# Optimization experiments

Measured on AMD Instinct MI355X. Metric: run time of the kernel, lower is better.

Reference implementation:

```python
import jax, jax.numpy as jnp
import numpy as np

B, NQ, NC1, NC2 = 2, 1024, 1024, 1024
QD = CD1 = CD2 = 1024
H, DH = 8, 64
INNER = H * DH          # 512
VD = 1024               # v_dim, split across heads -> 128 per head
VDH = VD // H


def setup_inputs() -> dict:
    key = jax.random.key(0)
    ks = jax.random.split(key, 18)
    f = lambda k, shape: jax.random.normal(k, shape, jnp.float32) * 0.02
    return {
        "x": f(ks[0], (B, NQ, QD)),
        "context": f(ks[1], (B, NC1, CD1)),
        "context2": f(ks[2], (B, NC2, CD2)),
        "mask1": jax.random.uniform(ks[3], (B, NQ, NC1)) > 0.1,
        "mask2": jax.random.uniform(ks[4], (B, NQ, NC2)) > 0.1,
        "Wq": f(ks[5], (QD, INNER)),  "bq": f(ks[6], (INNER,)),
        "Wk1": f(ks[7], (CD1, INNER)), "bk1": f(ks[8], (INNER,)),
        "Wv1": f(ks[9], (CD1, VD)),    "bv1": f(ks[10], (VD,)),
        "Wk2": f(ks[11], (CD2, INNER)), "bk2": f(ks[12], (INNER,)),
        "Wv2": f(ks[13], (CD2, VD)),    "bv2": f(ks[14], (VD,)),
        "Wo": f(ks[15], (VD, VD)),      "bo": f(ks[16], (VD,)),
    }


def _split_heads(t, d):
    # b n (h d) -> b h n d
    b, n, _ = t.shape
    return t.reshape(b, n, H, d).transpose(0, 2, 1, 3)


def reference(x, context, context2, mask1, mask2,
              Wq, bq, Wk1, bk1, Wv1, bv1, Wk2, bk2, Wv2, bv2, Wo, bo):
    scale = DH ** -0.5
    q = x @ Wq + bq
    k = jnp.concatenate([context @ Wk1 + bk1, context2 @ Wk2 + bk2], axis=1)
    v = jnp.concatenate([context @ Wv1 + bv1, context2 @ Wv2 + bv2], axis=1)

    qh = _split_heads(q, DH)   # [B,H,NQ,DH]
    kh = _split_heads(k, DH)   # [B,H,NC1+NC2,DH]
    vh = _split_heads(v, VDH)  # [B,H,NC1+NC2,VDH]

    sim = jnp.einsum('bhid,bhjd->bhij', qh, kh) * scale  # [B,H,NQ,J]
    mask = jnp.concatenate([mask1, mask2], axis=2)[:, None, :, :]  # [B,1,NQ,J]
    max_neg = -jnp.finfo(sim.dtype).max
    sim = jnp.where(mask, sim, max_neg)

    attn = jax.nn.softmax(sim, axis=-1)
    out = jnp.einsum('bhij,bhjd->bhid', attn, vh)          # [B,H,NQ,VDH]
    out = out.transpose(0, 2, 1, 3).reshape(B, NQ, VD)     # b n (h d)
    return out @ Wo + bo
```

## Files before the change

kernel.cpp:

```cpp
#include <hip/hip_runtime.h>
#include <math.h>

typedef short bf16x8 __attribute__((ext_vector_type(8)));
typedef float f32x4  __attribute__((ext_vector_type(4)));

__device__ __forceinline__ unsigned short f2bf(float f) {
    unsigned int u = __builtin_bit_cast(unsigned int, f);
    u += 0x7FFFu + ((u >> 16) & 1u);
    return (unsigned short)(u >> 16);
}
__device__ __forceinline__ float bf2f(unsigned short u) {
    return __builtin_bit_cast(float, (unsigned int)u << 16);
}
__device__ __forceinline__ unsigned pktrunc(float hi, float lo) {
    return __builtin_amdgcn_perm(__builtin_bit_cast(unsigned, hi),
                                 __builtin_bit_cast(unsigned, lo), 0x07060302u);
}

__device__ __forceinline__ void gld16(const unsigned short* g, unsigned short* l) {
    __builtin_amdgcn_global_load_lds(
        (const __attribute__((address_space(1))) void*)g,
        (__attribute__((address_space(3))) void*)l, 16, 0, 0);
}

#define QSCALE 0.18033688011112042f

__global__ __launch_bounds__(256) void prep(
    const float* __restrict__ x, const float* __restrict__ c1, const float* __restrict__ c2,
    const int* __restrict__ mask1, const int* __restrict__ mask2,
    const float* __restrict__ Wq, const float* __restrict__ Wk1, const float* __restrict__ Wk2,
    const float* __restrict__ Wv1, const float* __restrict__ Wv2, const float* __restrict__ Wo,
    unsigned short* __restrict__ xb, unsigned short* __restrict__ c1b, unsigned short* __restrict__ c2b,
    unsigned short* __restrict__ Wqt, unsigned short* __restrict__ Wk1t, unsigned short* __restrict__ Wk2t,
    unsigned short* __restrict__ Wv1t, unsigned short* __restrict__ Wv2t, unsigned short* __restrict__ Wot,
    unsigned long long* __restrict__ mpk)
{
    __shared__ float T[64][65];
    const int bid = blockIdx.x, t = threadIdx.x;

    if (bid < 3072) {
        const int z = bid >> 10;
        const float* a = z == 0 ? x : (z == 1 ? c1 : c2);
        unsigned short* o = z == 0 ? xb : (z == 1 ? c1b : c2b);
        size_t i = ((size_t)(bid & 1023) * 256 + t) * 8;
        float4 x0 = *(const float4*)&a[i];
        float4 x1 = *(const float4*)&a[i + 4];
        uint4 pk;
        pk.x = (unsigned)f2bf(x0.x) | ((unsigned)f2bf(x0.y) << 16);
        pk.y = (unsigned)f2bf(x0.z) | ((unsigned)f2bf(x0.w) << 16);
        pk.z = (unsigned)f2bf(x1.x) | ((unsigned)f2bf(x1.y) << 16);
        pk.w = (unsigned)f2bf(x1.z) | ((unsigned)f2bf(x1.w) << 16);
        *(uint4*)&o[i] = pk;
        return;
    }
    if (bid < 4224) {
        const float* W; unsigned short* O; int N, n0, k0; bool perm = false;
        if (bid < 3456) {
            int l = bid - 3072, z = l >> 7, rem = l & 127;
            W = z == 0 ? Wq : (z == 1 ? Wk1 : Wk2);
            O = z == 0 ? Wqt : (z == 1 ? Wk1t : Wk2t);
            N = 512; n0 = (rem & 7) << 6; k0 = (rem >> 3) << 6;
        } else {
            int l = bid - 3456, z = l >> 8, rem = l & 255;
            W = z == 0 ? Wv1 : (z == 1 ? Wv2 : Wo);
            O = z == 0 ? Wv1t : (z == 1 ? Wv2t : Wot);
            N = 1024; n0 = (rem & 15) << 6; k0 = (rem >> 4) << 6;
            perm = (z == 2);
        }
        #pragma unroll
        for (int i = 0; i < 4; i++) {
            int vi = t + (i << 8);
            int r = vi >> 4, c4 = (vi & 15) << 2;
            *(float4*)&T[r][c4] = *(const float4*)&W[(size_t)(k0 + r) * N + n0 + c4];
        }
        __syncthreads();
        #pragma unroll
        for (int i = 0; i < 4; i++) {
            int vi = t + (i << 8);
            int n = vi >> 4, k4 = (vi & 15) << 2;
            if (!perm) {
                uint2 pk;
                pk.x = (unsigned)f2bf(T[k4 + 0][n]) | ((unsigned)f2bf(T[k4 + 1][n]) << 16);
                pk.y = (unsigned)f2bf(T[k4 + 2][n]) | ((unsigned)f2bf(T[k4 + 3][n]) << 16);
                *(uint2*)&O[(size_t)(n0 + n) * 1024 + k0 + k4] = pk;
            } else {
                #pragma unroll
                for (int ii = 0; ii < 4; ii++) {
                    int k = k0 + k4 + ii, f = k & 127;
                    int kp = (k & ~127) | ((f & 15) << 3) | (f >> 4);
                    O[(size_t)(n0 + n) * 1024 + kp] = f2bf(T[k4 + ii][n]);
                }
            }
        }
        return;
    }
    {
        int wid = ((bid - 4224) << 2) + (t >> 6);
        int lane = t & 63;
        const int* m1 = mask1 + ((size_t)wid << 10);
        const int* m2 = mask2 + ((size_t)wid << 10);
        unsigned long long* o = mpk + ((size_t)wid << 5);
        #pragma unroll
        for (int win = 0; win < 16; win++) {
            unsigned long long bal = __ballot(m1[(win << 6) + lane] != 0);
            if (lane == 0) o[win] = bal;
        }
        #pragma unroll
        for (int win = 0; win < 16; win++) {
            unsigned long long bal = __ballot(m2[(win << 6) + lane] != 0);
            if (lane == 0) o[16 + win] = bal;
        }
    }
}

template<int NT>
__device__ __forceinline__ void gemm_core(
    const unsigned short* __restrict__ A,
    const unsigned short* __restrict__ Wt,
    int K, int gm0, int gn0,
    unsigned short (*As)[32], unsigned short (*Bs)[32],
    f32x4 (&acc)[4][NT / 32])
{
    constexpr int NS = NT / 32;
    const int t = threadIdx.x;
    const int lane = t & 63, w = t >> 6;
    const int wm = (w & 1) << 6, wn = (w >> 1) * (NT / 2);
    const int l15 = lane & 15, quad = lane >> 4;

    for (int k0 = 0; k0 < K; k0 += 32) {
        __syncthreads();
        #pragma unroll
        for (int i = 0; i < 2; i++) {
            int r0 = (i << 6) + (w << 4);
            int ra = r0 + (lane >> 2);
            int kc = (lane & 3) << 3;
            gld16(&A[(size_t)(gm0 + ra) * K + k0 + kc], &As[r0][0] + ((size_t)lane << 3));
        }
        #pragma unroll
        for (int i = 0; i < NT / 64; i++) {
            int r0 = (i << 6) + (w << 4);
            int ra = r0 + (lane >> 2);
            int kc = (lane & 3) << 3;
            gld16(&Wt[(size_t)(gn0 + ra) * K + k0 + kc], &Bs[r0][0] + ((size_t)lane << 3));
        }
        __syncthreads();
        bf16x8 af[4], bg[NS];
        #pragma unroll
        for (int i = 0; i < 4; i++)
            af[i] = *(const bf16x8*)&As[wm + (i << 4) + l15][quad << 3];
        #pragma unroll
        for (int j = 0; j < NS; j++)
            bg[j] = *(const bf16x8*)&Bs[wn + (j << 4) + l15][quad << 3];
        #pragma unroll
        for (int i = 0; i < 4; i++)
            #pragma unroll
            for (int j = 0; j < NS; j++)
                acc[i][j] = __builtin_amdgcn_mfma_f32_16x16x32_bf16(af[i], bg[j], acc[i][j], 0, 0, 0);
    }
}

__global__ __launch_bounds__(256) void proj_all(
    const unsigned short* __restrict__ xb, const unsigned short* __restrict__ c1b,
    const unsigned short* __restrict__ c2b,
    const unsigned short* __restrict__ Wqt, const unsigned short* __restrict__ Wk1t,
    const unsigned short* __restrict__ Wk2t, const unsigned short* __restrict__ Wv1t,
    const unsigned short* __restrict__ Wv2t,
    const float* __restrict__ bq, const float* __restrict__ bk1, const float* __restrict__ bk2,
    const float* __restrict__ bv1, const float* __restrict__ bv2,
    unsigned short* __restrict__ qbuf, unsigned short* __restrict__ khb,
    unsigned short* __restrict__ vhb)
{
    __shared__ unsigned short smem[17408];
    unsigned short (*As)[32] = (unsigned short(*)[32])smem;
    unsigned short (*Bs)[32] = (unsigned short(*)[32])(smem + 4096);
    unsigned short* Ts = smem;

    const int bid = blockIdx.x;
    int z, bx, by;
    if (bid < 192) { z = bid >> 6; int l = bid & 63; by = l >> 2; bx = l & 3; }
    else { int l = bid - 192; z = 3 + (l >> 7); l &= 127; by = l >> 3; bx = l & 7; }
    const unsigned short* A  = (z == 0) ? xb : (z == 1 || z == 3) ? c1b : c2b;
    const unsigned short* Wt = (z == 0) ? Wqt : (z == 1) ? Wk1t : (z == 2) ? Wk2t
                             : (z == 3) ? Wv1t : Wv2t;
    const float* bias = (z == 0) ? bq : (z == 1) ? bk1 : (z == 2) ? bk2
                      : (z == 3) ? bv1 : bv2;
    const int gm0 = by << 7, gn0 = bx << 7;

    f32x4 acc[4][4];
    #pragma unroll
    for (int i = 0; i < 4; i++)
        #pragma unroll
        for (int j = 0; j < 4; j++) acc[i][j] = (f32x4){0.f, 0.f, 0.f, 0.f};

    gemm_core<128>(A, Wt, 1024, gm0, gn0, As, Bs, acc);

    const int t = threadIdx.x;
    const int lane = t & 63, w = t >> 6;
    const int wm = (w & 1) << 6, wn = (w >> 1) << 6;
    const int l15 = lane & 15, quad = lane >> 4;
    float bb[4];
    #pragma unroll
    for (int j = 0; j < 4; j++) bb[j] = bias[gn0 + wn + (j << 4) + l15];

    if (z == 0) {
        #pragma unroll
        for (int i = 0; i < 4; i++) {
            int mb = gm0 + wm + (i << 4) + (quad << 2);
            #pragma unroll
            for (int p = 0; p < 4; p++)
                #pragma unroll
                for (int j = 0; j < 4; j++)
                    qbuf[(size_t)(mb + p) * 512 + gn0 + wn + (j << 4) + l15]
                        = f2bf((acc[i][j][p] + bb[j]) * QSCALE);
        }
        return;
    }

    __syncthreads();
    const int b = gm0 >> 10;
    if (z < 3) {
        const int jb = ((z == 2) ? 1024 : 0) + (gm0 & 1023);
        #pragma unroll
        for (int i = 0; i < 4; i++) {
            int jl0 = wm + (i << 4) + (quad << 2);
            #pragma unroll
            for (int j = 0; j < 4; j++) {
                int n = wn + (j << 4) + l15;
                #pragma unroll
                for (int p = 0; p < 4; p++)
                    Ts[(jl0 + p) * 136 + n] = f2bf(acc[i][j][p] + bb[j]);
            }
        }
        __syncthreads();
        #pragma unroll
        for (int rr = 0; rr < 8; rr++) {
            int row = (rr << 4) + (t >> 4), cd = t & 15;
            uint4 v = *(const uint4*)&Ts[row * 136 + (cd << 3)];
            int jg = jb + row;
            int hcol = (gn0 >> 6) + (cd >> 3);
            size_t hb = ((size_t)((b << 3) + hcol) << 17);
            *(uint4*)&khb[hb + ((size_t)jg << 6) + ((((cd & 7) ^ (jg & 7))) << 3)] = v;
        }
    } else {
        const int jb = ((z == 3) ? 0 : 1024) + (gm0 & 1023);
        #pragma unroll
        for (int i = 0; i < 4; i++) {
            int jl0 = wm + (i << 4) + (quad << 2);
            #pragma unroll
            for (int j = 0; j < 4; j++) {
                int n = wn + (j << 4) + l15;
                unsigned long long pk = 0;
                #pragma unroll
                for (int p = 0; p < 4; p++)
                    pk |= (unsigned long long)f2bf(acc[i][j][p] + bb[j]) << (16 * p);
                *(unsigned long long*)&Ts[n * 136 + jl0] = pk;
            }
        }
        __syncthreads();
        const int hv = gn0 >> 7;
        size_t hbase = ((size_t)((b << 3) + hv) << 18);
        #pragma unroll
        for (int rr = 0; rr < 8; rr++) {
            int f = (rr << 4) + (t >> 4), cj = t & 15;
            uint4 v = *(const uint4*)&Ts[f * 136 + (cj << 3)];
            int jj = jb + (cj << 3);
            int jpos = (jj & ~63) | ((((jj >> 3) & 7) ^ (f & 7)) << 3);
            *(uint4*)&vhb[hbase + ((size_t)f << 11) + jpos] = v;
        }
    }
}

__global__ __launch_bounds__(256) void gemm_out(
    const unsigned short* __restrict__ abuf, const unsigned short* __restrict__ Wot,
    const float* __restrict__ bo, float* __restrict__ out)
{
    __shared__ unsigned short As[128][32];
    __shared__ unsigned short Bs[64][32];
    const int gm0 = blockIdx.y << 7, gn0 = blockIdx.x << 6;

    f32x4 acc[4][2];
    #pragma unroll
    for (int i = 0; i < 4; i++)
        #pragma unroll
        for (int j = 0; j < 2; j++) acc[i][j] = (f32x4){0.f, 0.f, 0.f, 0.f};

    gemm_core<64>(abuf, Wot, 1024, gm0, gn0, As, Bs, acc);

    const int lane = threadIdx.x & 63, w = threadIdx.x >> 6;
    const int wm = (w & 1) << 6, wn = (w >> 1) << 5;
    const int l15 = lane & 15, quad = lane >> 4;
    float bb[2];
    #pragma unroll
    for (int j = 0; j < 2; j++) bb[j] = bo[gn0 + wn + (j << 4) + l15];
    #pragma unroll
    for (int i = 0; i < 4; i++) {
        int mb = gm0 + wm + (i << 4) + (quad << 2);
        #pragma unroll
        for (int p = 0; p < 4; p++)
            #pragma unroll
            for (int j = 0; j < 2; j++)
                out[(size_t)(mb + p) * 1024 + gn0 + wn + (j << 4) + l15] = acc[i][j][p] + bb[j];
    }
}

__global__ __launch_bounds__(256) void attn_mfma(
    const unsigned short* __restrict__ qbuf, const unsigned short* __restrict__ khb,
    const unsigned short* __restrict__ vhb, const unsigned long long* __restrict__ mpk,
    unsigned short* __restrict__ Opart, float* __restrict__ ml)
{
    __shared__ unsigned short Ks[64 * 64];
    __shared__ unsigned short VsT[128 * 64];
    __shared__ unsigned short Ps[64 * 64];

    const int t = threadIdx.x;
    const int bid = blockIdx.x;
    const int hs = bid >> 8, r = bid & 255;
    const int h = r & 7, qt = (r >> 3) & 15, b = r >> 7;
    const int q0 = qt << 6;
    const int lane = t & 63, w = t >> 6, l15 = lane & 15, quad = lane >> 4;
    const int v7 = l15 & 7;

    const unsigned short* qrow = qbuf + (((size_t)(b << 10) + q0 + (w << 4) + l15) << 9) + (h << 6);
    const bf16x8 aq0 = *(const bf16x8*)&qrow[quad << 3];
    const bf16x8 aq1 = *(const bf16x8*)&qrow[32 + (quad << 3)];

    f32x4 acc[8];
    #pragma unroll
    for (int ct = 0; ct < 8; ct++) acc[ct] = (f32x4){0.f, 0.f, 0.f, 0.f};
    float m_l = -3.0e38f, l_l = 0.f;

    const unsigned short* kh = khb + ((size_t)((b << 3) + h) << 17);
    const unsigned short* vh = vhb + ((size_t)((b << 3) + h) << 18);
    const unsigned long long* mrow = mpk + (((size_t)(b << 10) + q0 + (w << 4) + l15) << 5) + (hs << 3);
    const int prow = ((w << 4) + l15) << 6;

    for (int jt = 0; jt < 8; jt++) {
        const int j0 = (hs << 9) + (jt << 6);
        __syncthreads();
        {
            const unsigned short* kg = kh + ((size_t)j0 << 6);
            int o = (w << 10) + (lane << 3);
            gld16(kg + o, Ks + o);
            gld16(kg + o + 512, Ks + o + 512);
        }
        #pragma unroll
        for (int it = 0; it < 4; it++) {
            int f0 = (w << 5) + (it << 3);
            gld16(vh + ((size_t)(f0 + (lane >> 3)) << 11) + j0 + ((lane & 7) << 3),
                  VsT + (f0 << 6) + (lane << 3));
        }
        __syncthreads();

        const unsigned long long mw = mrow[jt];

        f32x4 s[4];
        #pragma unroll
        for (int n = 0; n < 4; n++) {
            int rowk = (n << 4) + l15;
            bf16x8 bk0 = *(const bf16x8*)&Ks[(rowk << 6) + ((quad ^ v7) << 3)];
            bf16x8 bk1 = *(const bf16x8*)&Ks[(rowk << 6) + (((quad + 4) ^ v7) << 3)];
            s[n] = (f32x4){0.f, 0.f, 0.f, 0.f};
            s[n] = __builtin_amdgcn_mfma_f32_16x16x32_bf16(bk0, aq0, s[n], 0, 0, 0);
            s[n] = __builtin_amdgcn_mfma_f32_16x16x32_bf16(bk1, aq1, s[n], 0, 0, 0);
        }
        #pragma unroll
        for (int n = 0; n < 4; n++)
            #pragma unroll
            for (int p = 0; p < 4; p++)
                s[n][p] = ((mw >> ((n << 4) + (quad << 2) + p)) & 1ull) ? s[n][p] : -3.0e38f;

        float mt = s[0][0];
        #pragma unroll
        for (int n = 0; n < 4; n++)
            #pragma unroll
            for (int p = 0; p < 4; p++) mt = fmaxf(mt, s[n][p]);
        mt = fmaxf(mt, __shfl_xor(mt, 16, 64));
        mt = fmaxf(mt, __shfl_xor(mt, 32, 64));
        float mn = fmaxf(m_l, mt);
        float ls = 0.f;
        #pragma unroll
        for (int n = 0; n < 4; n++) {
            float e0 = __builtin_amdgcn_exp2f(s[n][0] - mn);
            float e1 = __builtin_amdgcn_exp2f(s[n][1] - mn);
            float e2 = __builtin_amdgcn_exp2f(s[n][2] - mn);
            float e3 = __builtin_amdgcn_exp2f(s[n][3] - mn);
            ls += (e0 + e1) + (e2 + e3);
            uint2 pk;
            pk.x = pktrunc(e1, e0);
            pk.y = pktrunc(e3, e2);
            int mblk = ((n << 1) + (quad >> 1)) ^ v7;
            *(uint2*)&Ps[prow + (mblk << 3) + ((quad & 1) << 2)] = pk;
        }
        ls += __shfl_xor(ls, 16, 64);
        ls += __shfl_xor(ls, 32, 64);
        float al = __builtin_amdgcn_exp2f(m_l - mn);
        l_l = l_l * al + ls;
        m_l = mn;

        float ar[4];
        #pragma unroll
        for (int p = 0; p < 4; p++)
            ar[p] = __shfl(al, (lane & 48) | ((quad << 2) + p), 64);
        #pragma unroll
        for (int ct = 0; ct < 8; ct++)
            #pragma unroll
            for (int p = 0; p < 4; p++) acc[ct][p] *= ar[p];

        bf16x8 ap[2];
        #pragma unroll
        for (int win = 0; win < 2; win++) {
            int mblk = ((win << 2) + quad) ^ v7;
            ap[win] = *(const bf16x8*)&Ps[prow + (mblk << 3)];
        }
        #pragma unroll
        for (int ct = 0; ct < 8; ct++) {
            int f = (ct << 4) + l15;
            #pragma unroll
            for (int win = 0; win < 2; win++) {
                int c = (win << 2) + quad;
                bf16x8 bv = *(const bf16x8*)&VsT[(f << 6) + ((c ^ v7) << 3)];
                acc[ct] = __builtin_amdgcn_mfma_f32_16x16x32_bf16(ap[win], bv, acc[ct], 0, 0, 0);
            }
        }
    }

    #pragma unroll
    for (int p = 0; p < 4; p++) {
        int q = q0 + (w << 4) + (quad << 2) + p;
        size_t idx = ((size_t)hs << 14) + ((size_t)((b << 3) + h) << 10) + q;
        uint4 pk;
        pk.x = (unsigned)f2bf(acc[0][p]) | ((unsigned)f2bf(acc[1][p]) << 16);
        pk.y = (unsigned)f2bf(acc[2][p]) | ((unsigned)f2bf(acc[3][p]) << 16);
        pk.z = (unsigned)f2bf(acc[4][p]) | ((unsigned)f2bf(acc[5][p]) << 16);
        pk.w = (unsigned)f2bf(acc[6][p]) | ((unsigned)f2bf(acc[7][p]) << 16);
        *(uint4*)&Opart[(idx << 7) + (l15 << 3)] = pk;
    }
    if (quad == 0) {
        int q = q0 + (w << 4) + l15;
        size_t idx = ((size_t)hs << 14) + ((size_t)((b << 3) + h) << 10) + q;
        ml[(idx << 1) + 0] = m_l;
        ml[(idx << 1) + 1] = l_l;
    }
}

__global__ __launch_bounds__(256) void attn_combine(
    const unsigned short* __restrict__ Opart, const float* __restrict__ ml,
    unsigned short* __restrict__ abuf)
{
    int id = (blockIdx.x << 8) + threadIdx.x;
    int bhq = id >> 5, c = id & 31;
    float2 m0 = ((const float2*)ml)[bhq];
    float2 m1 = ((const float2*)ml)[16384 + bhq];
    float2 m2 = ((const float2*)ml)[32768 + bhq];
    float2 m3 = ((const float2*)ml)[49152 + bhq];
    float M = fmaxf(fmaxf(m0.x, m1.x), fmaxf(m2.x, m3.x));
    float a0 = __builtin_amdgcn_exp2f(m0.x - M), a1 = __builtin_amdgcn_exp2f(m1.x - M);
    float a2 = __builtin_amdgcn_exp2f(m2.x - M), a3 = __builtin_amdgcn_exp2f(m3.x - M);
    float inv = 1.0f / (m0.y * a0 + m1.y * a1 + m2.y * a2 + m3.y * a3);
    a0 *= inv; a1 *= inv; a2 *= inv; a3 *= inv;
    float o[4] = {0.f, 0.f, 0.f, 0.f};
    float as[4] = {a0, a1, a2, a3};
    #pragma unroll
    for (int s = 0; s < 4; s++) {
        uint2 v = *(const uint2*)&Opart[((size_t)(s * 16384 + bhq) << 7) + (c << 2)];
        o[0] += as[s] * bf2f((unsigned short)(v.x & 0xFFFF));
        o[1] += as[s] * bf2f((unsigned short)(v.x >> 16));
        o[2] += as[s] * bf2f((unsigned short)(v.y & 0xFFFF));
        o[3] += as[s] * bf2f((unsigned short)(v.y >> 16));
    }
    int b = bhq >> 13, hh = (bhq >> 10) & 7, q = bhq & 1023;
    unsigned long long pk = (unsigned long long)f2bf(o[0])
        | ((unsigned long long)f2bf(o[1]) << 16)
        | ((unsigned long long)f2bf(o[2]) << 32)
        | ((unsigned long long)f2bf(o[3]) << 48);
    *(unsigned long long*)&abuf[((size_t)((b << 10) + q) << 10) + (hh << 7) + (c << 2)] = pk;
}

extern "C" void kernel_launch(void* const* d_in, const int* in_sizes, int n_in,
                              void* d_out, int out_size, void* d_ws, size_t ws_size,
                              hipStream_t stream)
{
    const float* x        = (const float*)d_in[0];
    const float* context  = (const float*)d_in[1];
    const float* context2 = (const float*)d_in[2];
    const int*   mask1    = (const int*)d_in[3];
    const int*   mask2    = (const int*)d_in[4];
    const float* Wq  = (const float*)d_in[5];
    const float* bq  = (const float*)d_in[6];
    const float* Wk1 = (const float*)d_in[7];
    const float* bk1 = (const float*)d_in[8];
    const float* Wv1 = (const float*)d_in[9];
    const float* bv1 = (const float*)d_in[10];
    const float* Wk2 = (const float*)d_in[11];
    const float* bk2 = (const float*)d_in[12];
    const float* Wv2 = (const float*)d_in[13];
    const float* bv2 = (const float*)d_in[14];
    const float* Wo  = (const float*)d_in[15];
    const float* bo  = (const float*)d_in[16];
    float* out = (float*)d_out;

    char* W = (char*)d_ws;
    unsigned short* Wot  = (unsigned short*)(W);
    unsigned short* xb   = (unsigned short*)(W + (2ull  << 20));
    unsigned short* c1b  = (unsigned short*)(W + (6ull  << 20));
    unsigned short* c2b  = (unsigned short*)(W + (10ull << 20));
    unsigned short* Wqt  = (unsigned short*)(W + (14ull << 20));
    unsigned short* Wk1t = (unsigned short*)(W + (15ull << 20));
    unsigned short* Wk2t = (unsigned short*)(W + (16ull << 20));
    unsigned short* Wv1t = (unsigned short*)(W + (17ull << 20));
    unsigned short* Wv2t = (unsigned short*)(W + (19ull << 20));
    unsigned short* qbuf = (unsigned short*)(W + (21ull << 20));
    unsigned short* khb  = (unsigned short*)(W + (23ull << 20));
    unsigned short* vhb  = (unsigned short*)(W + (27ull << 20));
    unsigned long long* mpk = (unsigned long long*)(W + (35ull << 20));
    float*          mlb  = (float*)(W + (35ull << 20) + (1ull << 19));
    unsigned short* Opart = (unsigned short*)(W + (2ull << 20));
    unsigned short* abuf  = (unsigned short*)(W + (19ull << 20));

    prep<<<dim3(4736), 256, 0, stream>>>(x, context, context2, mask1, mask2,
                                         Wq, Wk1, Wk2, Wv1, Wv2, Wo,
                                         xb, c1b, c2b, Wqt, Wk1t, Wk2t, Wv1t, Wv2t, Wot, mpk);
    proj_all<<<dim3(448), 256, 0, stream>>>(xb, c1b, c2b, Wqt, Wk1t, Wk2t, Wv1t, Wv2t,
                                            bq, bk1, bk2, bv1, bv2, qbuf, khb, vhb);
    attn_mfma<<<dim3(1024), 256, 0, stream>>>(qbuf, khb, vhb, mpk, Opart, mlb);
    attn_combine<<<dim3(2048), 256, 0, stream>>>(Opart, mlb, abuf);
    gemm_out<<<dim3(16, 16), 256, 0, stream>>>(abuf, Wot, bo, out);
}
```

Measured before the change: 219.9 us.

## Fuse split-KV combine into attention via last-block counter; widen GEMM K-tile with swizzle

The separate attn_combine kernel is removed. The last of the four KV-split blocks for each row tile, detected with an atomic counter and thread fences, now merges the partial outputs and writes abuf. This saves one launch and a pass over global memory, at the cost of a memset and some atomic and fence overhead. The shared GEMM core now loads a 64-wide K slice per step with an XOR-swizzled LDS layout, halving the number of barriers and reducing bank conflicts. The attention kernel also prefetches the next mask word and adds a launch-bounds occupancy hint.

After: 339.5 us. +54.4%, slower.

```diff
diff --git a/kernel.cpp b/kernel.cpp
--- a/kernel.cpp
+++ b/kernel.cpp
@@ -114,48 +114,55 @@
 }
 
 template<int NT>
-__device__ __forceinline__ void gemm_core(
+__device__ __forceinline__ void gemm_core64(
     const unsigned short* __restrict__ A,
     const unsigned short* __restrict__ Wt,
     int K, int gm0, int gn0,
-    unsigned short (*As)[32], unsigned short (*Bs)[32],
+    unsigned short* As, unsigned short* Bs,
     f32x4 (&acc)[4][NT / 32])
 {
-    constexpr int NS = NT / 32;
     const int t = threadIdx.x;
     const int lane = t & 63, w = t >> 6;
     const int wm = (w & 1) << 6, wn = (w >> 1) * (NT / 2);
     const int l15 = lane & 15, quad = lane >> 4;
-
-    for (int k0 = 0; k0 < K; k0 += 32) {
-        __syncthreads();
-        #pragma unroll
-        for (int i = 0; i < 2; i++) {
-            int r0 = (i << 6) + (w << 4);
-            int ra = r0 + (lane >> 2);
-            int kc = (lane & 3) << 3;
-            gld16(&A[(size_t)(gm0 + ra) * K + k0 + kc], &As[r0][0] + ((size_t)lane << 3));
-        }
-        #pragma unroll
-        for (int i = 0; i < NT / 64; i++) {
-            int r0 = (i << 6) + (w << 4);
-            int ra = r0 + (lane >> 2);
-            int kc = (lane & 3) << 3;
-            gld16(&Wt[(size_t)(gn0 + ra) * K + k0 + kc], &Bs[r0][0] + ((size_t)lane << 3));
-        }
-        __syncthreads();
-        bf16x8 af[4], bg[NS];
-        #pragma unroll
-        for (int i = 0; i < 4; i++)
-            af[i] = *(const bf16x8*)&As[wm + (i << 4) + l15][quad << 3];
-        #pragma unroll
-        for (int j = 0; j < NS; j++)
-            bg[j] = *(const bf16x8*)&Bs[wn + (j << 4) + l15][quad << 3];
-        #pragma unroll
-        for (int i = 0; i < 4; i++)
-            #pragma unroll
-            for (int j = 0; j < NS; j++)
-                acc[i][j] = __builtin_amdgcn_mfma_f32_16x16x32_bf16(af[i], bg[j], acc[i][j], 0, 0, 0);
+    const int lrow = lane >> 3, lchk = lane & 7;
+
+    for (int k0 = 0; k0 < K; k0 += 64) {
+        __syncthreads();
+        #pragma unroll
+        for (int i = 0; i < 4; i++) {
+            int r0 = (w << 5) + (i << 3);
+            int ra = r0 + lrow;
+            int kc = (lchk ^ (ra & 7)) << 3;
+            gld16(&A[(size_t)(gm0 + ra) * K + k0 + kc], As + (r0 << 6) + (lane << 3));
+        }
+        #pragma unroll
+        for (int i = 0; i < NT / 32; i++) {
+            int r0 = w * (NT >> 2) + (i << 3);
+            int ra = r0 + lrow;
+            int kc = (lchk ^ (ra & 7)) << 3;
+            gld16(&Wt[(size_t)(gn0 + ra) * K + k0 + kc], Bs + (r0 << 6) + (lane << 3));
+        }
+        __syncthreads();
+        #pragma unroll
+        for (int kk = 0; kk < 2; kk++) {
+            bf16x8 af[4], bg[NT / 32];
+            #pragma unroll
+            for (int i = 0; i < 4; i++) {
+                int row = wm + (i << 4) + l15;
+                af[i] = *(const bf16x8*)&As[(row << 6) + ((((kk << 2) + quad) ^ (row & 7)) << 3)];
+            }
+            #pragma unroll
+            for (int j = 0; j < NT / 32; j++) {
+                int row = wn + (j << 4) + l15;
+                bg[j] = *(const bf16x8*)&Bs[(row << 6) + ((((kk << 2) + quad) ^ (row & 7)) << 3)];
+            }
+            #pragma unroll
+            for (int i = 0; i < 4; i++)
+                #pragma unroll
+                for (int j = 0; j < NT / 32; j++)
+                    acc[i][j] = __builtin_amdgcn_mfma_f32_16x16x32_bf16(af[i], bg[j], acc[i][j], 0, 0, 0);
+        }
     }
 }
 
@@ -171,8 +178,8 @@
     unsigned short* __restrict__ vhb)
 {
     __shared__ unsigned short smem[17408];
-    unsigned short (*As)[32] = (unsigned short(*)[32])smem;
-    unsigned short (*Bs)[32] = (unsigned short(*)[32])(smem + 4096);
+    unsigned short* As = smem;
+    unsigned short* Bs = smem + 8192;
     unsigned short* Ts = smem;
 
     const int bid = blockIdx.x;
@@ -192,7 +199,7 @@
         #pragma unroll
         for (int j = 0; j < 4; j++) acc[i][j] = (f32x4){0.f, 0.f, 0.f, 0.f};
 
-    gemm_core<128>(A, Wt, 1024, gm0, gn0, As, Bs, acc);
+    gemm_core64<128>(A, Wt, 1024, gm0, gn0, As, Bs, acc);
 
     const int t = threadIdx.x;
     const int lane = t & 63, w = t >> 6;
@@ -274,8 +281,9 @@
     const unsigned short* __restrict__ abuf, const unsigned short* __restrict__ Wot,
     const float* __restrict__ bo, float* __restrict__ out)
 {
-    __shared__ unsigned short As[128][32];
-    __shared__ unsigned short Bs[64][32];
+    __shared__ unsigned short smem[12288];
+    unsigned short* As = smem;
+    unsigned short* Bs = smem + 8192;
     const int gm0 = blockIdx.y << 7, gn0 = blockIdx.x << 6;
 
     f32x4 acc[4][2];
@@ -284,7 +292,7 @@
         #pragma unroll
         for (int j = 0; j < 2; j++) acc[i][j] = (f32x4){0.f, 0.f, 0.f, 0.f};
 
-    gemm_core<64>(abuf, Wot, 1024, gm0, gn0, As, Bs, acc);
+    gemm_core64<64>(abuf, Wot, 1024, gm0, gn0, As, Bs, acc);
 
     const int lane = threadIdx.x & 63, w = threadIdx.x >> 6;
     const int wm = (w & 1) << 6, wn = (w >> 1) << 5;
@@ -303,14 +311,16 @@
     }
 }
 
-__global__ __launch_bounds__(256) void attn_mfma(
+__global__ __launch_bounds__(256, 4) void attn_mfma(
     const unsigned short* __restrict__ qbuf, const unsigned short* __restrict__ khb,
     const unsigned short* __restrict__ vhb, const unsigned long long* __restrict__ mpk,
-    unsigned short* __restrict__ Opart, float* __restrict__ ml)
+    unsigned short* __restrict__ Opart, float* __restrict__ ml,
+    int* __restrict__ cnt, unsigned short* __restrict__ abuf)
 {
     __shared__ unsigned short Ks[64 * 64];
     __shared__ unsigned short VsT[128 * 64];
     __shared__ unsigned short Ps[64 * 64];
+    __shared__ int winner_sh;
 
     const int t = threadIdx.x;
     const int bid = blockIdx.x;
@@ -334,6 +344,8 @@
     const unsigned long long* mrow = mpk + (((size_t)(b << 10) + q0 + (w << 4) + l15) << 5) + (hs << 3);
     const int prow = ((w << 4) + l15) << 6;
 
+    unsigned long long mw = mrow[0];
+
     for (int jt = 0; jt < 8; jt++) {
         const int j0 = (hs << 9) + (jt << 6);
         __syncthreads();
@@ -351,7 +363,7 @@
         }
         __syncthreads();
 
-        const unsigned long long mw = mrow[jt];
+        unsigned long long mw_nxt = mrow[(jt + 1) & 7];
 
         f32x4 s[4];
         #pragma unroll
@@ -368,6 +380,7 @@
             #pragma unroll
             for (int p = 0; p < 4; p++)
                 s[n][p] = ((mw >> ((n << 4) + (quad << 2) + p)) & 1ull) ? s[n][p] : -3.0e38f;
+        mw = mw_nxt;
 
         float mt = s[0][0];
         #pragma unroll
@@ -424,10 +437,11 @@
         }
     }
 
+    const size_t bh10 = (size_t)((b << 3) + h) << 10;
     #pragma unroll
     for (int p = 0; p < 4; p++) {
         int q = q0 + (w << 4) + (quad << 2) + p;
-        size_t idx = ((size_t)hs << 14) + ((size_t)((b << 3) + h) << 10) + q;
+        size_t idx = ((size_t)hs << 14) + bh10 + q;
         uint4 pk;
         pk.x = (unsigned)f2bf(acc[0][p]) | ((unsigned)f2bf(acc[1][p]) << 16);
         pk.y = (unsigned)f2bf(acc[2][p]) | ((unsigned)f2bf(acc[3][p]) << 16);
@@ -437,43 +451,47 @@
     }
     if (quad == 0) {
         int q = q0 + (w << 4) + l15;
-        size_t idx = ((size_t)hs << 14) + ((size_t)((b << 3) + h) << 10) + q;
+        size_t idx = ((size_t)hs << 14) + bh10 + q;
         ml[(idx << 1) + 0] = m_l;
         ml[(idx << 1) + 1] = l_l;
     }
-}
-
-__global__ __launch_bounds__(256) void attn_combine(
-    const unsigned short* __restrict__ Opart, const float* __restrict__ ml,
-    unsigned short* __restrict__ abuf)
-{
-    int id = (blockIdx.x << 8) + threadIdx.x;
-    int bhq = id >> 5, c = id & 31;
-    float2 m0 = ((const float2*)ml)[bhq];
-    float2 m1 = ((const float2*)ml)[16384 + bhq];
-    float2 m2 = ((const float2*)ml)[32768 + bhq];
-    float2 m3 = ((const float2*)ml)[49152 + bhq];
-    float M = fmaxf(fmaxf(m0.x, m1.x), fmaxf(m2.x, m3.x));
-    float a0 = __builtin_amdgcn_exp2f(m0.x - M), a1 = __builtin_amdgcn_exp2f(m1.x - M);
-    float a2 = __builtin_amdgcn_exp2f(m2.x - M), a3 = __builtin_amdgcn_exp2f(m3.x - M);
-    float inv = 1.0f / (m0.y * a0 + m1.y * a1 + m2.y * a2 + m3.y * a3);
-    a0 *= inv; a1 *= inv; a2 *= inv; a3 *= inv;
-    float o[4] = {0.f, 0.f, 0.f, 0.f};
-    float as[4] = {a0, a1, a2, a3};
-    #pragma unroll
-    for (int s = 0; s < 4; s++) {
-        uint2 v = *(const uint2*)&Opart[((size_t)(s * 16384 + bhq) << 7) + (c << 2)];
-        o[0] += as[s] * bf2f((unsigned short)(v.x & 0xFFFF));
-        o[1] += as[s] * bf2f((unsigned short)(v.x >> 16));
-        o[2] += as[s] * bf2f((unsigned short)(v.y & 0xFFFF));
-        o[3] += as[s] * bf2f((unsigned short)(v.y >> 16));
-    }
-    int b = bhq >> 13, hh = (bhq >> 10) & 7, q = bhq & 1023;
-    unsigned long long pk = (unsigned long long)f2bf(o[0])
-        | ((unsigned long long)f2bf(o[1]) << 16)
-        | ((unsigned long long)f2bf(o[2]) << 32)
-        | ((unsigned long long)f2bf(o[3]) << 48);
-    *(unsigned long long*)&abuf[((size_t)((b << 10) + q) << 10) + (hh << 7) + (c << 2)] = pk;
+
+    __threadfence();
+    __syncthreads();
+    if (t == 0) winner_sh = (atomicAdd(&cnt[r], 1) == 3) ? 1 : 0;
+    __syncthreads();
+    if (!winner_sh) return;
+    __threadfence();
+
+    #pragma unroll
+    for (int it = 0; it < 8; it++) {
+        int id = (it << 8) + t;
+        int q = q0 + (id >> 5), c = id & 31;
+        size_t idx0 = bh10 + q;
+        float2 m0 = *(const float2*)&ml[(idx0)          << 1];
+        float2 m1 = *(const float2*)&ml[(idx0 + 16384)  << 1];
+        float2 m2 = *(const float2*)&ml[(idx0 + 32768)  << 1];
+        float2 m3 = *(const float2*)&ml[(idx0 + 49152)  << 1];
+        float M = fmaxf(fmaxf(m0.x, m1.x), fmaxf(m2.x, m3.x));
+        float a0 = __builtin_amdgcn_exp2f(m0.x - M), a1 = __builtin_amdgcn_exp2f(m1.x - M);
+        float a2 = __builtin_amdgcn_exp2f(m2.x - M), a3 = __builtin_amdgcn_exp2f(m3.x - M);
+        float inv = 1.0f / (m0.y * a0 + m1.y * a1 + m2.y * a2 + m3.y * a3);
+        float as[4] = {a0 * inv, a1 * inv, a2 * inv, a3 * inv};
+        float o[4] = {0.f, 0.f, 0.f, 0.f};
+        #pragma unroll
+        for (int s = 0; s < 4; s++) {
+            uint2 v = *(const uint2*)&Opart[((idx0 + (size_t)s * 16384) << 7) + (c << 2)];
+            o[0] += as[s] * bf2f((unsigned short)(v.x & 0xFFFF));
+            o[1] += as[s] * bf2f((unsigned short)(v.x >> 16));
+            o[2] += as[s] * bf2f((unsigned short)(v.y & 0xFFFF));
+            o[3] += as[s] * bf2f((unsigned short)(v.y >> 16));
+        }
+        unsigned long long pk = (unsigned long long)f2bf(o[0])
+            | ((unsigned long long)f2bf(o[1]) << 16)
+            | ((unsigned long long)f2bf(o[2]) << 32)
+            | ((unsigned long long)f2bf(o[3]) << 48);
+        *(unsigned long long*)&abuf[((size_t)((b << 10) + q) << 10) + (h << 7) + (c << 2)] = pk;
+    }
 }
 
 extern "C" void kernel_launch(void* const* d_in, const int* in_sizes, int n_in,
@@ -514,15 +532,16 @@
     unsigned short* vhb  = (unsigned short*)(W + (27ull << 20));
     unsigned long long* mpk = (unsigned long long*)(W + (35ull << 20));
     float*          mlb  = (float*)(W + (35ull << 20) + (1ull << 19));
+    int*            cnt  = (int*)(W + (36ull << 20));
     unsigned short* Opart = (unsigned short*)(W + (2ull << 20));
     unsigned short* abuf  = (unsigned short*)(W + (19ull << 20));
 
+    hipMemsetAsync(cnt, 0, 1024, stream);
     prep<<<dim3(4736), 256, 0, stream>>>(x, context, context2, mask1, mask2,
                                          Wq, Wk1, Wk2, Wv1, Wv2, Wo,
                                          xb, c1b, c2b, Wqt, Wk1t, Wk2t, Wv1t, Wv2t, Wot, mpk);
     proj_all<<<dim3(448), 256, 0, stream>>>(xb, c1b, c2b, Wqt, Wk1t, Wk2t, Wv1t, Wv2t,
                                             bq, bk1, bk2, bv1, bv2, qbuf, khb, vhb);
-    attn_mfma<<<dim3(1024), 256, 0, stream>>>(qbuf, khb, vhb, mpk, Opart, mlb);
-    attn_combine<<<dim3(2048), 256, 0, stream>>>(Opart, mlb, abuf);
+    attn_mfma<<<dim3(1024), 256, 0, stream>>>(qbuf, khb, vhb, mpk, Opart, mlb, cnt, abuf);
     gemm_out<<<dim3(16, 16), 256, 0, stream>>>(abuf, Wot, bo, out);
 }
```
